# Optimization experiments

Measured on AMD Instinct MI355X. Metric: run time of the kernel, lower is better.

## Reference

```python
import jax, jax.numpy as jnp
import numpy as np

IN_DIM, OUT_DIM, HIDDEN = 64, 64, 128


def _cell(x, h, c, w_ih, w_hh, b_ih, b_hh):
    # PyTorch LSTM gate order: i, f, g, o
    gates = x @ w_ih.T + b_ih + h @ w_hh.T + b_hh
    i, f, g, o = jnp.split(gates, 4, axis=-1)
    c = jax.nn.sigmoid(f) * c + jax.nn.sigmoid(i) * jnp.tanh(g)
    h = jax.nn.sigmoid(o) * jnp.tanh(c)
    return h, c


def setup_inputs() -> dict:
    key = jax.random.key(0)
    ks = jax.random.split(key, 12)
    B, S = 8192, 128
    s = 1.0 / np.sqrt(HIDDEN)
    u = lambda k, shp: jax.random.uniform(k, shp, jnp.float32, -s, s)
    return {
        "x": jax.random.normal(ks[0], (B, S, IN_DIM), jnp.float32),
        "w_ih0": u(ks[1], (4 * HIDDEN, IN_DIM)),
        "w_hh0": u(ks[2], (4 * HIDDEN, HIDDEN)),
        "b_ih0": u(ks[3], (4 * HIDDEN,)),
        "b_hh0": u(ks[4], (4 * HIDDEN,)),
        "w_ih1": u(ks[5], (4 * HIDDEN, HIDDEN)),
        "w_hh1": u(ks[6], (4 * HIDDEN, HIDDEN)),
        "b_ih1": u(ks[7], (4 * HIDDEN,)),
        "b_hh1": u(ks[8], (4 * HIDDEN,)),
        "w_dec": u(ks[9], (OUT_DIM, HIDDEN)),
        "b_dec": u(ks[10], (OUT_DIM,)),
        "pred_steps": 20,
    }


def reference(x, w_ih0, w_hh0, b_ih0, b_hh0, w_ih1, w_hh1, b_ih1, b_hh1, w_dec, b_dec, pred_steps):
    B = x.shape[0]
    z = jnp.zeros((B, HIDDEN), x.dtype)

    def enc_step(carry, xt):
        h0, c0, h1, c1 = carry
        h0, c0 = _cell(xt, h0, c0, w_ih0, w_hh0, b_ih0, b_hh0)
        h1, c1 = _cell(h0, h1, c1, w_ih1, w_hh1, b_ih1, b_hh1)
        return (h0, c0, h1, c1), None

    carry, _ = jax.lax.scan(enc_step, (z, z, z, z), jnp.swapaxes(x, 0, 1))

    def dec_step(carry, _):
        inp, h0, c0, h1, c1 = carry
        h0, c0 = _cell(inp, h0, c0, w_ih0, w_hh0, b_ih0, b_hh0)
        h1, c1 = _cell(h0, h1, c1, w_ih1, w_hh1, b_ih1, b_hh1)
        p = h1 @ w_dec.T + b_dec
        return (p, h0, c0, h1, c1), p

    _, preds = jax.lax.scan(dec_step, (x[:, -1, :],) + carry, None, length=pred_steps)
    return jnp.swapaxes(preds, 0, 1)  # [B, pred_steps, out_dim]
```

## Files before the change

### kernel.cpp

```cpp
#include <hip/hip_runtime.h>
#include <cstdint>
#include <cstddef>

#define BATCH  8192
#define INDIM  64
#define OUTDIM 64
#define HID    128
#define BT     64
#define NT     512
#define KP     328
#define COLH0  64
#define COLH1  192
#define KB0    6
#define KB1    8
#define KBD    4

#define W0U    0
#define W1U    196608
#define WDU    458752
#define B0F    237568
#define B1F    238080
#define BDF    238592
#define NPACK  238656

typedef unsigned short u16;
typedef __attribute__((ext_vector_type(8))) short bfrag;
typedef __attribute__((ext_vector_type(4))) float facc;

__device__ __forceinline__ u16 f2bf(float x) {
  uint32_t u = __float_as_uint(x);
  return (u16)((u + 0x7fffu + ((u >> 16) & 1u)) >> 16);
}
__device__ __forceinline__ float bf2f(u16 h) {
  return __uint_as_float(((uint32_t)h) << 16);
}
__device__ __forceinline__ float fsig(float x) { return 1.0f / (1.0f + __expf(-x)); }
__device__ __forceinline__ float ftanh(float x) {
  float e = __expf(2.0f * x);
  return 1.0f - 2.0f / (e + 1.0f);
}
__device__ __forceinline__ facc splat4(float v) {
  facc a; a[0] = v; a[1] = v; a[2] = v; a[3] = v; return a;
}

__device__ __forceinline__ void loadw8(bfrag (&dst)[8], const u16* __restrict__ wt,
                                       int ntq, int kbn, int kb) {
#pragma unroll
  for (int t = 0; t < 4; ++t) {
    const u16* p = wt + (((ntq + t) * kbn + kb) * 2) * 512;
    dst[t * 2]     = *(const bfrag*)p;
    dst[t * 2 + 1] = *(const bfrag*)(p + 512);
  }
}

__device__ __forceinline__ void mfma_kb(const bfrag (&wf)[8],
                                        const u16 (&Hhi)[BT][KP],
                                        const u16 (&Hlo)[BT][KP],
                                        int k0, int c, facc (&acc)[4][4]) {
#pragma unroll
  for (int mt = 0; mt < 4; ++mt) {
    const bfrag ah = *(const bfrag*)&Hhi[mt * 16 + c][k0];
    const bfrag al = *(const bfrag*)&Hlo[mt * 16 + c][k0];
#pragma unroll
    for (int t = 0; t < 4; ++t) {
      facc a = acc[mt][t];
      a = __builtin_amdgcn_mfma_f32_16x16x32_bf16(ah, wf[t * 2],     a, 0, 0, 0);
      a = __builtin_amdgcn_mfma_f32_16x16x32_bf16(ah, wf[t * 2 + 1], a, 0, 0, 0);
      a = __builtin_amdgcn_mfma_f32_16x16x32_bf16(al, wf[t * 2],     a, 0, 0, 0);
      acc[mt][t] = a;
    }
  }
}

template <int KB>
__device__ __forceinline__ void gemm_phase(const u16* __restrict__ wt,
                                           const u16* __restrict__ wtNext, int kbnNext,
                                           const u16 (&Hhi)[BT][KP],
                                           const u16 (&Hlo)[BT][KP],
                                           int colOff, int c, int gk, int ntq,
                                           bfrag (&bufA)[8], bfrag (&bufB)[8],
                                           facc (&acc)[4][4]) {
  static_assert((KB & 1) == 0, "KB must be even");
#pragma unroll
  for (int kb = 0; kb < KB; kb += 2) {
    loadw8(bufB, wt, ntq, KB, kb + 1);
    mfma_kb(bufA, Hhi, Hlo, colOff + kb * 32 + gk, c, acc);
    if (kb + 2 < KB) loadw8(bufA, wt, ntq, KB, kb + 2);
    else             loadw8(bufA, wtNext, ntq, kbnNext, 0);
    mfma_kb(bufB, Hhi, Hlo, colOff + (kb + 1) * 32 + gk, c, acc);
  }
}

__global__ __launch_bounds__(NT, 2) void lstm_kernel(
    const float* __restrict__ x, const void* __restrict__ pkv,
    float* __restrict__ out, int S, int P) {
  __shared__ __align__(16) u16 Ahi[BT][KP];
  __shared__ __align__(16) u16 Alo[BT][KP];

  const u16* pku = (const u16*)pkv;
  const float* pkf = (const float*)pkv;

  const int tid = threadIdx.x;
  const int lane = tid & 63;
  const int w = tid >> 6;
  const int c = lane & 15;
  const int gk = (lane >> 4) * 8;
  const int g = lane >> 4;
  const int ntq = w * 4;
  const int b0 = blockIdx.x * BT;

  for (int i = tid; i < BT * KP; i += NT) {
    (&Ahi[0][0])[i] = 0;
    (&Alo[0][0])[i] = 0;
  }

  float b0r[4], b1r[4];
#pragma unroll
  for (int t = 0; t < 4; ++t) {
    b0r[t] = pkf[B0F + (w * 4 + t) * 16 + c];
    b1r[t] = pkf[B1F + (w * 4 + t) * 16 + c];
  }
  const int ntd = w & 3, mtd = w >> 2;
  const float bdr = pkf[BDF + ntd * 16 + c];

  float c0r[16], c1r[16];
#pragma unroll
  for (int q = 0; q < 16; ++q) { c0r[q] = 0.f; c1r[q] = 0.f; }

  const u16* w0t = pku + W0U + lane * 8;
  const u16* w1t = pku + W1U + lane * 8;
  const u16* wdt = pku + WDU + lane * 8;

  bfrag bufA[8], bufB[8];
  loadw8(bufA, w0t, ntq, KB0, 0);

  __syncthreads();

  const int T = S + P;
  for (int step = 0; step < T; ++step) {
    if (step < S) {
#pragma unroll
      for (int i = 0; i < 2; ++i) {
        const int q = tid + NT * i;
        const int s = q >> 4, c4 = (q & 15) * 4;
        const float4 v = *(const float4*)(x + ((size_t)(b0 + s) * S + step) * INDIM + c4);
        float vv[4] = {v.x, v.y, v.z, v.w};
        u16 h4[4], l4[4];
#pragma unroll
        for (int qq = 0; qq < 4; ++qq) {
          h4[qq] = f2bf(vv[qq]);
          l4[qq] = f2bf(vv[qq] - bf2f(h4[qq]));
        }
        uint2 hp, lp;
        hp.x = (uint32_t)h4[0] | ((uint32_t)h4[1] << 16);
        hp.y = (uint32_t)h4[2] | ((uint32_t)h4[3] << 16);
        lp.x = (uint32_t)l4[0] | ((uint32_t)l4[1] << 16);
        lp.y = (uint32_t)l4[2] | ((uint32_t)l4[3] << 16);
        *(uint2*)&Ahi[s][c4] = hp;
        *(uint2*)&Alo[s][c4] = lp;
      }
    }
    __syncthreads();

    facc acc[4][4];
#pragma unroll
    for (int mt = 0; mt < 4; ++mt)
#pragma unroll
      for (int t = 0; t < 4; ++t) acc[mt][t] = splat4(b0r[t]);
    gemm_phase<KB0>(w0t, w1t, KB1, Ahi, Alo, 0, c, gk, ntq, bufA, bufB, acc);
    __syncthreads();
#pragma unroll
    for (int mt = 0; mt < 4; ++mt)
#pragma unroll
      for (int r = 0; r < 4; ++r) {
        float gi = fsig(acc[mt][0][r]);
        float gf = fsig(acc[mt][1][r]);
        float gg = ftanh(acc[mt][2][r]);
        float go = fsig(acc[mt][3][r]);
        float cn = fmaf(gf, c0r[mt * 4 + r], gi * gg);
        c0r[mt * 4 + r] = cn;
        float hv = go * ftanh(cn);
        const int s = mt * 16 + g * 4 + r;
        u16 hh = f2bf(hv);
        Ahi[s][COLH0 + w * 16 + c] = hh;
        Alo[s][COLH0 + w * 16 + c] = f2bf(hv - bf2f(hh));
      }
    __syncthreads();

#pragma unroll
    for (int mt = 0; mt < 4; ++mt)
#pragma unroll
      for (int t = 0; t < 4; ++t) acc[mt][t] = splat4(b1r[t]);
    gemm_phase<KB1>(w1t, w0t, KB0, Ahi, Alo, COLH0, c, gk, ntq, bufA, bufB, acc);
    __syncthreads();
#pragma unroll
    for (int mt = 0; mt < 4; ++mt)
#pragma unroll
      for (int r = 0; r < 4; ++r) {
        float gi = fsig(acc[mt][0][r]);
        float gf = fsig(acc[mt][1][r]);
        float gg = ftanh(acc[mt][2][r]);
        float go = fsig(acc[mt][3][r]);
        float cn = fmaf(gf, c1r[mt * 4 + r], gi * gg);
        c1r[mt * 4 + r] = cn;
        float hv = go * ftanh(cn);
        const int s = mt * 16 + g * 4 + r;
        u16 hh = f2bf(hv);
        Ahi[s][COLH1 + w * 16 + c] = hh;
        Alo[s][COLH1 + w * 16 + c] = f2bf(hv - bf2f(hh));
      }

    if (step >= S) {
      bfrag wdf[8];
#pragma unroll
      for (int kb = 0; kb < KBD; ++kb) {
        const u16* p = wdt + ((ntd * KBD + kb) * 2) * 512;
        wdf[kb * 2]     = *(const bfrag*)p;
        wdf[kb * 2 + 1] = *(const bfrag*)(p + 512);
      }
      __syncthreads();
      facc da[2] = {splat4(bdr), splat4(bdr)};
#pragma unroll
      for (int kb = 0; kb < KBD; ++kb) {
        const int k0 = COLH1 + kb * 32 + gk;
#pragma unroll
        for (int mi = 0; mi < 2; ++mi) {
          const int mt = mtd + mi * 2;
          bfrag dah = *(const bfrag*)&Ahi[mt * 16 + c][k0];
          bfrag dal = *(const bfrag*)&Alo[mt * 16 + c][k0];
          da[mi] = __builtin_amdgcn_mfma_f32_16x16x32_bf16(dah, wdf[kb * 2],     da[mi], 0, 0, 0);
          da[mi] = __builtin_amdgcn_mfma_f32_16x16x32_bf16(dah, wdf[kb * 2 + 1], da[mi], 0, 0, 0);
          da[mi] = __builtin_amdgcn_mfma_f32_16x16x32_bf16(dal, wdf[kb * 2],     da[mi], 0, 0, 0);
        }
      }
      const int dstep = step - S;
#pragma unroll
      for (int mi = 0; mi < 2; ++mi) {
        const int mt = mtd + mi * 2;
#pragma unroll
        for (int r = 0; r < 4; ++r) {
          const int s = mt * 16 + g * 4 + r;
          const int o = ntd * 16 + c;
          float pv = da[mi][r];
          out[((size_t)(b0 + s) * P + dstep) * OUTDIM + o] = pv;
          u16 hh = f2bf(pv);
          Ahi[s][o] = hh;
          Alo[s][o] = f2bf(pv - bf2f(hh));
        }
      }
    }
  }
}

__global__ void prepack_kernel(const float* __restrict__ wih0, const float* __restrict__ whh0,
                               const float* __restrict__ bih0, const float* __restrict__ bhh0,
                               const float* __restrict__ wih1, const float* __restrict__ whh1,
                               const float* __restrict__ bih1, const float* __restrict__ bhh1,
                               const float* __restrict__ wdec, const float* __restrict__ bdec,
                               void* __restrict__ pko) {
  int idx = blockIdx.x * blockDim.x + threadIdx.x;
  if (idx >= NPACK) return;
  u16* pu = (u16*)pko;
  float* pf = (float*)pko;
  if (idx < 98304) {
    int nt = idx / 3072, rem = idx % 3072;
    int kb = rem >> 9, q = rem & 511, ln = q >> 3, j = q & 7;
    int n = nt * 16 + (ln & 15);
    int row = ((n >> 4) & 3) * HID + (n >> 6) * 16 + (n & 15);
    int k = kb * 32 + (ln >> 4) * 8 + j;
    float wv = (k < INDIM) ? wih0[row * INDIM + k] : whh0[row * HID + k - INDIM];
    u16 hi = f2bf(wv), lo = f2bf(wv - bf2f(hi));
    int base = W0U + ((nt * KB0 + kb) * 2) * 512;
    pu[base + q] = hi;
    pu[base + 512 + q] = lo;
  } else if (idx < 229376) {
    int r = idx - 98304;
    int nt = r >> 12, rem = r & 4095;
    int kb = rem >> 9, q = rem & 511, ln = q >> 3, j = q & 7;
    int n = nt * 16 + (ln & 15);
    int row = ((n >> 4) & 3) * HID + (n >> 6) * 16 + (n & 15);
    int k = kb * 32 + (ln >> 4) * 8 + j;
    float wv = (k < HID) ? wih1[row * HID + k] : whh1[row * HID + k - HID];
    u16 hi = f2bf(wv), lo = f2bf(wv - bf2f(hi));
    int base = W1U + ((nt * KB1 + kb) * 2) * 512;
    pu[base + q] = hi;
    pu[base + 512 + q] = lo;
  } else if (idx < 237568) {
    int r = idx - 229376;
    int nt = r >> 11, rem = r & 2047;
    int kb = rem >> 9, q = rem & 511, ln = q >> 3, j = q & 7;
    int o = nt * 16 + (ln & 15);
    int k = kb * 32 + (ln >> 4) * 8 + j;
    float wv = wdec[o * HID + k];
    u16 hi = f2bf(wv), lo = f2bf(wv - bf2f(hi));
    int base = WDU + ((nt * KBD + kb) * 2) * 512;
    pu[base + q] = hi;
    pu[base + 512 + q] = lo;
  } else if (idx < 238080) {
    int n = idx - 237568;
    int row = ((n >> 4) & 3) * HID + (n >> 6) * 16 + (n & 15);
    pf[B0F + n] = bih0[row] + bhh0[row];
  } else if (idx < 238592) {
    int n = idx - 238080;
    int row = ((n >> 4) & 3) * HID + (n >> 6) * 16 + (n & 15);
    pf[B1F + n] = bih1[row] + bhh1[row];
  } else {
    int o = idx - 238592;
    pf[BDF + o] = bdec[o];
  }
}

extern "C" void kernel_launch(void* const* d_in, const int* in_sizes, int n_in,
                              void* d_out, int out_size, void* d_ws, size_t ws_size,
                              hipStream_t stream) {
  const float* x    = (const float*)d_in[0];
  const float* wih0 = (const float*)d_in[1];
  const float* whh0 = (const float*)d_in[2];
  const float* bih0 = (const float*)d_in[3];
  const float* bhh0 = (const float*)d_in[4];
  const float* wih1 = (const float*)d_in[5];
  const float* whh1 = (const float*)d_in[6];
  const float* bih1 = (const float*)d_in[7];
  const float* bhh1 = (const float*)d_in[8];
  const float* wdec = (const float*)d_in[9];
  const float* bdec = (const float*)d_in[10];
  float* out = (float*)d_out;

  const int S = in_sizes[0] / (BATCH * INDIM);
  const int P = out_size / (BATCH * OUTDIM);

  prepack_kernel<<<(NPACK + 255) / 256, 256, 0, stream>>>(
      wih0, whh0, bih0, bhh0, wih1, whh1, bih1, bhh1, wdec, bdec, d_ws);

  lstm_kernel<<<BATCH / BT, NT, 0, stream>>>(x, d_ws, out, S, P);
}
```

Baseline: 5.538 ms.

## Prefetch next-step input into registers and use LDS-only barriers

Loads of x for the next timestep are issued into registers right after the layer-0 GEMM, so their global latency is hidden behind the activation and layer-1 work instead of sitting at the top of each step. Every __syncthreads is replaced by a custom barrier that waits only on LDS counters (lgkmcnt), so in-flight global loads such as weight prefetches and the x prefetch do not stall the barrier. Launch bounds drop from 2 to 1 block per CU, which gives the compiler more registers to hold the prefetched data but may lower occupancy. The LDS-only barrier depends on no global data being needed across it without an explicit wait.

```diff
diff --git a/kernel.cpp b/kernel.cpp
--- a/kernel.cpp
+++ b/kernel.cpp
@@ -43,6 +43,13 @@
   facc a; a[0] = v; a[1] = v; a[2] = v; a[3] = v; return a;
 }
 
+__device__ __forceinline__ void bar_lds() {
+  __builtin_amdgcn_sched_barrier(0);
+  asm volatile("s_waitcnt lgkmcnt(0)" ::: "memory");
+  __builtin_amdgcn_s_barrier();
+  __builtin_amdgcn_sched_barrier(0);
+}
+
 __device__ __forceinline__ void loadw8(bfrag (&dst)[8], const u16* __restrict__ wt,
                                        int ntq, int kbn, int kb) {
 #pragma unroll
@@ -91,7 +98,7 @@
   }
 }
 
-__global__ __launch_bounds__(NT, 2) void lstm_kernel(
+__global__ __launch_bounds__(NT, 1) void lstm_kernel(
     const float* __restrict__ x, const void* __restrict__ pkv,
     float* __restrict__ out, int S, int P) {
   __shared__ __align__(16) u16 Ahi[BT][KP];
@@ -134,7 +141,17 @@
   bfrag bufA[8], bufB[8];
   loadw8(bufA, w0t, ntq, KB0, 0);
 
-  __syncthreads();
+  float4 xr[2];
+  if (S > 0) {
+#pragma unroll
+    for (int i = 0; i < 2; ++i) {
+      const int q = tid + NT * i;
+      const int s = q >> 4, c4 = (q & 15) * 4;
+      xr[i] = *(const float4*)(x + (size_t)(b0 + s) * S * INDIM + c4);
+    }
+  }
+
+  bar_lds();
 
   const int T = S + P;
   for (int step = 0; step < T; ++step) {
@@ -143,8 +160,7 @@
       for (int i = 0; i < 2; ++i) {
         const int q = tid + NT * i;
         const int s = q >> 4, c4 = (q & 15) * 4;
-        const float4 v = *(const float4*)(x + ((size_t)(b0 + s) * S + step) * INDIM + c4);
-        float vv[4] = {v.x, v.y, v.z, v.w};
+        float vv[4] = {xr[i].x, xr[i].y, xr[i].z, xr[i].w};
         u16 h4[4], l4[4];
 #pragma unroll
         for (int qq = 0; qq < 4; ++qq) {
@@ -160,7 +176,7 @@
         *(uint2*)&Alo[s][c4] = lp;
       }
     }
-    __syncthreads();
+    bar_lds();
 
     facc acc[4][4];
 #pragma unroll
@@ -168,7 +184,17 @@
 #pragma unroll
       for (int t = 0; t < 4; ++t) acc[mt][t] = splat4(b0r[t]);
     gemm_phase<KB0>(w0t, w1t, KB1, Ahi, Alo, 0, c, gk, ntq, bufA, bufB, acc);
-    __syncthreads();
+    bar_lds();
+
+    if (step + 1 < S) {
+#pragma unroll
+      for (int i = 0; i < 2; ++i) {
+        const int q = tid + NT * i;
+        const int s = q >> 4, c4 = (q & 15) * 4;
+        xr[i] = *(const float4*)(x + ((size_t)(b0 + s) * S + step + 1) * INDIM + c4);
+      }
+    }
+
 #pragma unroll
     for (int mt = 0; mt < 4; ++mt)
 #pragma unroll
@@ -185,14 +211,14 @@
         Ahi[s][COLH0 + w * 16 + c] = hh;
         Alo[s][COLH0 + w * 16 + c] = f2bf(hv - bf2f(hh));
       }
-    __syncthreads();
+    bar_lds();
 
 #pragma unroll
     for (int mt = 0; mt < 4; ++mt)
 #pragma unroll
       for (int t = 0; t < 4; ++t) acc[mt][t] = splat4(b1r[t]);
     gemm_phase<KB1>(w1t, w0t, KB0, Ahi, Alo, COLH0, c, gk, ntq, bufA, bufB, acc);
-    __syncthreads();
+    bar_lds();
 #pragma unroll
     for (int mt = 0; mt < 4; ++mt)
 #pragma unroll
@@ -218,7 +244,7 @@
         wdf[kb * 2]     = *(const bfrag*)p;
         wdf[kb * 2 + 1] = *(const bfrag*)(p + 512);
       }
-      __syncthreads();
+      bar_lds();
       facc da[2] = {splat4(bdr), splat4(bdr)};
 #pragma unroll
       for (int kb = 0; kb < KBD; ++kb) {
```

After: 5.819 ms. 5.1% more time.
